# Optimization experiments

Measured on AMD Instinct MI355X. Metric: run time of the kernel, lower is better.

Reference implementation:

```python
import jax, jax.numpy as jnp
import numpy as np

BLOCK_NUM = 1024

def setup_inputs() -> dict:
    key = jax.random.key(0)
    k1, k2 = jax.random.split(key)
    regional_means = jax.random.normal(k1, (32, BLOCK_NUM, 128), dtype=jnp.float32)
    adj = jax.random.uniform(k2, (32, BLOCK_NUM, BLOCK_NUM), dtype=jnp.float32)
    return {"regional_means": regional_means, "adj": adj}

def reference(regional_means, adj):
    # Original: adj_means[b,i,j,f] = adj[b,i,j] * regional_means[b,j,f],
    # diagonal (i==j) zeroed, then summed over j.
    # Algebraically: (adj with zeroed diagonal) @ regional_means.
    n = adj.shape[-1]
    mask = 1.0 - jnp.eye(n, dtype=adj.dtype)  # (n, n)
    adj_masked = adj * mask  # (b, n, n)
    # (b, n, n) @ (b, n, f) -> (b, n, f)
    return jnp.einsum('bij,bjf->bif', adj_masked, regional_means)
```

## Files before the change

kernel.cpp:

```cpp
#include <hip/hip_runtime.h>
#include <hip/hip_bf16.h>
#include <stdint.h>

typedef __attribute__((ext_vector_type(4))) float f32x4;
typedef __attribute__((ext_vector_type(2))) float f32x2;
typedef __attribute__((ext_vector_type(8))) short short8;
typedef __attribute__((ext_vector_type(4))) unsigned int u32x4;

__device__ __forceinline__ unsigned short f2bf(float x) {
  __hip_bfloat16 h = __float2bfloat16(x);
  union { __hip_bfloat16 b; unsigned short s; } u; u.b = h;
  return u.s;
}
__device__ __forceinline__ unsigned int pkbf(float lo, float hi) {
  return (unsigned int)f2bf(lo) | ((unsigned int)f2bf(hi) << 16);
}
__device__ __forceinline__ f32x4 ld4(const float* p) { return *(const f32x4*)p; }


#define MSK(v, k) (((k) == arow) ? 0.f : (v))

#define LOADA(kt, Aa, Ab, Ac, Ad) do {                                  \
    const float* p_ = aP + (kt) * 64;                                   \
    Aa = ld4(p_); Ab = ld4(p_ + 4); Ac = ld4(p_ + 32); Ad = ld4(p_ + 36); \
  } while (0)

#define LOADB(kt, B_) do {                                              \
    const f32x2* p_ = (const f32x2*)(bP + (size_t)(kt) * 8192);         \
    _Pragma("unroll") for (int e_ = 0; e_ < 8; ++e_) B_[e_] = p_[e_ * 64]; \
  } while (0)

#define STAGEB(buf, B_) do {                                            \
    u32x4 ua_, ub_;                                                     \
    ua_[0] = pkbf(B_[0].x, B_[1].x); ua_[1] = pkbf(B_[2].x, B_[3].x);   \
    ua_[2] = pkbf(B_[4].x, B_[5].x); ua_[3] = pkbf(B_[6].x, B_[7].x);   \
    ub_[0] = pkbf(B_[0].y, B_[1].y); ub_[1] = pkbf(B_[2].y, B_[3].y);   \
    ub_[2] = pkbf(B_[4].y, B_[5].y); ub_[3] = pkbf(B_[6].y, B_[7].y);   \
    char* p_ = wP + (buf) * 16384;                                      \
    *(u32x4*)p_ = ua_; *(u32x4*)(p_ + 16) = ub_;                        \
  } while (0)

#define COMPUTE(buf, kt, Aa, Ab, Ac, Ad) do {                           \
    short8 af0_, af1_;                                                  \
    {                                                                   \
      union { u32x4 q; short8 s; } u0_, u1_;                            \
      if ((kt) == diag_kt) {  \
        const int jb_ = (kt) * 64 + kg;                                 \
        u0_.q[0] = pkbf(MSK(Aa[0], jb_ + 0),  MSK(Aa[1], jb_ + 1));     \
        u0_.q[1] = pkbf(MSK(Aa[2], jb_ + 2),  MSK(Aa[3], jb_ + 3));     \
        u0_.q[2] = pkbf(MSK(Ab[0], jb_ + 4),  MSK(Ab[1], jb_ + 5));     \
        u0_.q[3] = pkbf(MSK(Ab[2], jb_ + 6),  MSK(Ab[3], jb_ + 7));     \
        u1_.q[0] = pkbf(MSK(Ac[0], jb_ + 32), MSK(Ac[1], jb_ + 33));    \
        u1_.q[1] = pkbf(MSK(Ac[2], jb_ + 34), MSK(Ac[3], jb_ + 35));    \
        u1_.q[2] = pkbf(MSK(Ad[0], jb_ + 36), MSK(Ad[1], jb_ + 37));    \
        u1_.q[3] = pkbf(MSK(Ad[2], jb_ + 38), MSK(Ad[3], jb_ + 39));    \
      } else {                                                          \
        u0_.q[0] = pkbf(Aa[0], Aa[1]); u0_.q[1] = pkbf(Aa[2], Aa[3]);   \
        u0_.q[2] = pkbf(Ab[0], Ab[1]); u0_.q[3] = pkbf(Ab[2], Ab[3]);   \
        u1_.q[0] = pkbf(Ac[0], Ac[1]); u1_.q[1] = pkbf(Ac[2], Ac[3]);   \
        u1_.q[2] = pkbf(Ad[0], Ad[1]); u1_.q[3] = pkbf(Ad[2], Ad[3]);   \
      }                                                                 \
      af0_ = u0_.s; af1_ = u1_.s;                                       \
    }                                                                   \
    const char* base_ = rP + (buf) * 16384;                             \
    _Pragma("unroll")                                                   \
    for (int n_ = 0; n_ < 8; ++n_) {                                    \
      short8 bf0_ = *(const short8*)(base_ + (n_ * 2 + 0) * 1024);      \
      acc[n_] = __builtin_amdgcn_mfma_f32_16x16x32_bf16(af0_, bf0_, acc[n_], 0, 0, 0); \
      short8 bf1_ = *(const short8*)(base_ + (n_ * 2 + 1) * 1024);      \
      acc[n_] = __builtin_amdgcn_mfma_f32_16x16x32_bf16(af1_, bf1_, acc[n_], 0, 0, 0); \
    }                                                                   \
  } while (0)

__global__ __launch_bounds__(512) void gcn_kernel(
    const float* __restrict__ means, const float* __restrict__ adj,
    float* __restrict__ out) {
  __shared__ char ldsB[32768];

  const int tid = (int)threadIdx.x;
  const int l = tid & 63;
  const int w = tid >> 6;
  const int bid = (int)blockIdx.x;
  const int batch = (bid & 7) * 4 + (bid >> 6);
  const int rtile = (bid >> 3) & 7;
  const int rbase = rtile * 128;

  const float* aB = adj + (size_t)batch * 1048576;
  const float* mB = means + (size_t)batch * 131072;
  float* oB = out + (size_t)batch * 131072;

  const int arow = rbase + w * 16 + (l & 15);
  const int kg = (l >> 4) * 8;
  const float* aP = aB + (size_t)arow * 1024 + kg;
  const int diag_kt = arow >> 6;

  const int n_t = tid >> 6;
  const int s_t = (tid >> 5) & 1;
  const int g_t = (tid >> 3) & 3;
  const int fc_t = (tid & 7) * 2;
  const float* bP = mB + (size_t)(s_t * 32 + g_t * 8) * 128 + n_t * 16 + fc_t;

  char* wP = ldsB + tid * 32;
  const char* rP = ldsB + l * 16;

  f32x4 acc[8];
#pragma unroll
  for (int n = 0; n < 8; ++n) { f32x4 z = {0.f, 0.f, 0.f, 0.f}; acc[n] = z; }

  f32x4 A00, A01, A02, A03, A10, A11, A12, A13;
  f32x2 B0v[8], B1v[8];

  LOADA(0, A00, A01, A02, A03);
  LOADB(0, B0v);
  STAGEB(0, B0v);
  __syncthreads();

  for (int kt = 0; kt < 16; kt += 2) {
    LOADA(kt + 1, A10, A11, A12, A13);
    LOADB(kt + 1, B1v);
    COMPUTE(0, kt, A00, A01, A02, A03);
    STAGEB(1, B1v);
    __syncthreads();

    if (kt + 2 < 16) {
      LOADA(kt + 2, A00, A01, A02, A03);
      LOADB(kt + 2, B0v);
    }
    COMPUTE(1, kt + 1, A10, A11, A12, A13);
    if (kt + 2 < 16) STAGEB(0, B0v);
    __syncthreads();
  }

  const int orow = rbase + w * 16 + (l >> 4) * 4;
  const int ocol = l & 15;
  float* op = oB + (size_t)orow * 128 + ocol;
#pragma unroll
  for (int n = 0; n < 8; ++n)
#pragma unroll
    for (int j = 0; j < 4; ++j)
      op[j * 128 + n * 16] = acc[n][j];
}

extern "C" void kernel_launch(void* const* d_in, const int* in_sizes, int n_in,
                              void* d_out, int out_size, void* d_ws, size_t ws_size,
                              hipStream_t stream) {
  const float* means = (const float*)d_in[0];
  const float* adj = (const float*)d_in[1];
  float* out = (float*)d_out;
  hipLaunchKernelGGL(gcn_kernel, dim3(256), dim3(512), 0, stream, means, adj, out);
}
```

Before: 216.8 us.

## Halve row tile to 64 rows, 512 blocks, stage B in 128-k chunks

Cuts the row tile per block from 128 to 64 and the threads per block from 512 to 256, launching 512 blocks with launch bounds targeting two blocks per CU. The B operand (means) is staged into LDS in 128-deep k chunks across a 64KB double buffer, with one barrier per two k-steps instead of two per two. The aim is better CU fill on 256 CUs and less synchronisation, in exchange for each block re-reading the means matrix twice as often and doubling LDS use, which may limit occupancy.

After: 216.4 us. Within noise of the previous version (-0.2%).

```diff
diff --git a/kernel.cpp b/kernel.cpp
--- a/kernel.cpp
+++ b/kernel.cpp
@@ -20,70 +20,73 @@
 
 #define MSK(v, k) (((k) == arow) ? 0.f : (v))
 
-#define LOADA(kt, Aa, Ab, Ac, Ad) do {                                  \
-    const float* p_ = aP + (kt) * 64;                                   \
-    Aa = ld4(p_); Ab = ld4(p_ + 4); Ac = ld4(p_ + 32); Ad = ld4(p_ + 36); \
+#define LOADA(kt, Aq) do {                                               \
+    const float* p_ = aP + (kt) * 64;                                    \
+    Aq[0] = ld4(p_); Aq[1] = ld4(p_ + 4);                                \
+    Aq[2] = ld4(p_ + 32); Aq[3] = ld4(p_ + 36);                          \
   } while (0)
 
-#define LOADB(kt, B_) do {                                              \
-    const f32x2* p_ = (const f32x2*)(bP + (size_t)(kt) * 8192);         \
-    _Pragma("unroll") for (int e_ = 0; e_ < 8; ++e_) B_[e_] = p_[e_ * 64]; \
+#define STAGE_LOAD(q1, h, S_) do {                                       \
+    const float* p_ = bP0 + (q1) * 16384 + (h) * 4096;                   \
+    _Pragma("unroll") for (int e_ = 0; e_ < 8; ++e_)                     \
+      S_[e_] = *(const f32x2*)(p_ + e_ * 128);                           \
   } while (0)
 
-#define STAGEB(buf, B_) do {                                            \
-    u32x4 ua_, ub_;                                                     \
-    ua_[0] = pkbf(B_[0].x, B_[1].x); ua_[1] = pkbf(B_[2].x, B_[3].x);   \
-    ua_[2] = pkbf(B_[4].x, B_[5].x); ua_[3] = pkbf(B_[6].x, B_[7].x);   \
-    ub_[0] = pkbf(B_[0].y, B_[1].y); ub_[1] = pkbf(B_[2].y, B_[3].y);   \
-    ub_[2] = pkbf(B_[4].y, B_[5].y); ub_[3] = pkbf(B_[6].y, B_[7].y);   \
-    char* p_ = wP + (buf) * 16384;                                      \
-    *(u32x4*)p_ = ua_; *(u32x4*)(p_ + 16) = ub_;                        \
+#define STAGE_WRITE(nb, h, S_) do {                                      \
+    u32x4 ua_, ub_;                                                      \
+    ua_[0] = pkbf(S_[0].x, S_[1].x); ua_[1] = pkbf(S_[2].x, S_[3].x);    \
+    ua_[2] = pkbf(S_[4].x, S_[5].x); ua_[3] = pkbf(S_[6].x, S_[7].x);    \
+    ub_[0] = pkbf(S_[0].y, S_[1].y); ub_[1] = pkbf(S_[2].y, S_[3].y);    \
+    ub_[2] = pkbf(S_[4].y, S_[5].y); ub_[3] = pkbf(S_[6].y, S_[7].y);    \
+    char* p_ = wB + (nb) * 32768 + (h) * 1024;                           \
+    *(u32x4*)p_ = ua_; *(u32x4*)(p_ + 16) = ub_;                         \
   } while (0)
 
-#define COMPUTE(buf, kt, Aa, Ab, Ac, Ad) do {                           \
-    short8 af0_, af1_;                                                  \
-    {                                                                   \
-      union { u32x4 q; short8 s; } u0_, u1_;                            \
-      if ((kt) == diag_kt) {  \
-        const int jb_ = (kt) * 64 + kg;                                 \
-        u0_.q[0] = pkbf(MSK(Aa[0], jb_ + 0),  MSK(Aa[1], jb_ + 1));     \
-        u0_.q[1] = pkbf(MSK(Aa[2], jb_ + 2),  MSK(Aa[3], jb_ + 3));     \
-        u0_.q[2] = pkbf(MSK(Ab[0], jb_ + 4),  MSK(Ab[1], jb_ + 5));     \
-        u0_.q[3] = pkbf(MSK(Ab[2], jb_ + 6),  MSK(Ab[3], jb_ + 7));     \
-        u1_.q[0] = pkbf(MSK(Ac[0], jb_ + 32), MSK(Ac[1], jb_ + 33));    \
-        u1_.q[1] = pkbf(MSK(Ac[2], jb_ + 34), MSK(Ac[3], jb_ + 35));    \
-        u1_.q[2] = pkbf(MSK(Ad[0], jb_ + 36), MSK(Ad[1], jb_ + 37));    \
-        u1_.q[3] = pkbf(MSK(Ad[2], jb_ + 38), MSK(Ad[3], jb_ + 39));    \
-      } else {                                                          \
-        u0_.q[0] = pkbf(Aa[0], Aa[1]); u0_.q[1] = pkbf(Aa[2], Aa[3]);   \
-        u0_.q[2] = pkbf(Ab[0], Ab[1]); u0_.q[3] = pkbf(Ab[2], Ab[3]);   \
-        u1_.q[0] = pkbf(Ac[0], Ac[1]); u1_.q[1] = pkbf(Ac[2], Ac[3]);   \
-        u1_.q[2] = pkbf(Ad[0], Ad[1]); u1_.q[3] = pkbf(Ad[2], Ad[3]);   \
-      }                                                                 \
-      af0_ = u0_.s; af1_ = u1_.s;                                       \
-    }                                                                   \
-    const char* base_ = rP + (buf) * 16384;                             \
-    _Pragma("unroll")                                                   \
-    for (int n_ = 0; n_ < 8; ++n_) {                                    \
-      short8 bf0_ = *(const short8*)(base_ + (n_ * 2 + 0) * 1024);      \
+#define COMPUTE(buf, kt, Aq) do {                                        \
+    short8 af0_, af1_;                                                   \
+    {                                                                    \
+      union { u32x4 q; short8 s; } u0_, u1_;                             \
+      if ((kt) == diag_kt) {                                             \
+        const int jb_ = (kt) * 64 + kg;                                  \
+        u0_.q[0] = pkbf(MSK(Aq[0][0], jb_ + 0),  MSK(Aq[0][1], jb_ + 1)); \
+        u0_.q[1] = pkbf(MSK(Aq[0][2], jb_ + 2),  MSK(Aq[0][3], jb_ + 3)); \
+        u0_.q[2] = pkbf(MSK(Aq[1][0], jb_ + 4),  MSK(Aq[1][1], jb_ + 5)); \
+        u0_.q[3] = pkbf(MSK(Aq[1][2], jb_ + 6),  MSK(Aq[1][3], jb_ + 7)); \
+        u1_.q[0] = pkbf(MSK(Aq[2][0], jb_ + 32), MSK(Aq[2][1], jb_ + 33)); \
+        u1_.q[1] = pkbf(MSK(Aq[2][2], jb_ + 34), MSK(Aq[2][3], jb_ + 35)); \
+        u1_.q[2] = pkbf(MSK(Aq[3][0], jb_ + 36), MSK(Aq[3][1], jb_ + 37)); \
+        u1_.q[3] = pkbf(MSK(Aq[3][2], jb_ + 38), MSK(Aq[3][3], jb_ + 39)); \
+      } else {                                                           \
+        u0_.q[0] = pkbf(Aq[0][0], Aq[0][1]); u0_.q[1] = pkbf(Aq[0][2], Aq[0][3]); \
+        u0_.q[2] = pkbf(Aq[1][0], Aq[1][1]); u0_.q[3] = pkbf(Aq[1][2], Aq[1][3]); \
+        u1_.q[0] = pkbf(Aq[2][0], Aq[2][1]); u1_.q[1] = pkbf(Aq[2][2], Aq[2][3]); \
+        u1_.q[2] = pkbf(Aq[3][0], Aq[3][1]); u1_.q[3] = pkbf(Aq[3][2], Aq[3][3]); \
+      }                                                                  \
+      af0_ = u0_.s; af1_ = u1_.s;                                        \
+    }                                                                    \
+    const char* base_ = rP + (buf) * 32768;                              \
+    const int c_ = (kt) & 1;                                             \
+    _Pragma("unroll")                                                    \
+    for (int n_ = 0; n_ < 8; ++n_) {                                     \
+      short8 bf0_ = *(const short8*)(base_ + (n_ * 4 + 2 * c_ + 0) * 1024); \
       acc[n_] = __builtin_amdgcn_mfma_f32_16x16x32_bf16(af0_, bf0_, acc[n_], 0, 0, 0); \
-      short8 bf1_ = *(const short8*)(base_ + (n_ * 2 + 1) * 1024);      \
+      short8 bf1_ = *(const short8*)(base_ + (n_ * 4 + 2 * c_ + 1) * 1024); \
       acc[n_] = __builtin_amdgcn_mfma_f32_16x16x32_bf16(af1_, bf1_, acc[n_], 0, 0, 0); \
-    }                                                                   \
+    }                                                                    \
   } while (0)
 
-__global__ __launch_bounds__(512) void gcn_kernel(
+__global__ __launch_bounds__(256, 2) void gcn_kernel(
     const float* __restrict__ means, const float* __restrict__ adj,
     float* __restrict__ out) {
-  __shared__ char ldsB[32768];
+  __shared__ char ldsB[65536];
 
   const int tid = (int)threadIdx.x;
   const int l = tid & 63;
   const int w = tid >> 6;
   const int bid = (int)blockIdx.x;
-  const int batch = (bid & 7) * 4 + (bid >> 6);
-  const int rtile = (bid >> 3) & 7;
-  const int rbase = rtile * 128;
+  const int batch = (bid & 7) * 4 + (bid >> 7);
+  const int rtile = (bid >> 3) & 15;
+  const int rbase = rtile * 64;
 
   const float* aB = adj + (size_t)batch * 1048576;
   const float* mB = means + (size_t)batch * 131072;
@@ -94,41 +97,53 @@
   const float* aP = aB + (size_t)arow * 1024 + kg;
   const int diag_kt = arow >> 6;
 
-  const int n_t = tid >> 6;
-  const int s_t = (tid >> 5) & 1;
+  const int n_t = tid >> 5;
   const int g_t = (tid >> 3) & 3;
   const int fc_t = (tid & 7) * 2;
-  const float* bP = mB + (size_t)(s_t * 32 + g_t * 8) * 128 + n_t * 16 + fc_t;
-
-  char* wP = ldsB + tid * 32;
+  const float* bP0 = mB + (size_t)(g_t * 8) * 128 + n_t * 16 + fc_t;
+  char* wB = ldsB + n_t * 4096 + g_t * 256 + fc_t * 16;
   const char* rP = ldsB + l * 16;
 
   f32x4 acc[8];
 #pragma unroll
   for (int n = 0; n < 8; ++n) { f32x4 z = {0.f, 0.f, 0.f, 0.f}; acc[n] = z; }
 
-  f32x4 A00, A01, A02, A03, A10, A11, A12, A13;
-  f32x2 B0v[8], B1v[8];
+  f32x4 Ar[2][4];
 
-  LOADA(0, A00, A01, A02, A03);
-  LOADB(0, B0v);
-  STAGEB(0, B0v);
+  {
+    f32x2 S0[8], S1[8], S2[8], S3[8];
+    STAGE_LOAD(0, 0, S0); STAGE_LOAD(0, 1, S1);
+    STAGE_LOAD(0, 2, S2); STAGE_LOAD(0, 3, S3);
+    LOADA(0, Ar[0]);
+    STAGE_WRITE(0, 0, S0); STAGE_WRITE(0, 1, S1);
+    STAGE_WRITE(0, 2, S2); STAGE_WRITE(0, 3, S3);
+  }
   __syncthreads();
 
-  for (int kt = 0; kt < 16; kt += 2) {
-    LOADA(kt + 1, A10, A11, A12, A13);
-    LOADB(kt + 1, B1v);
-    COMPUTE(0, kt, A00, A01, A02, A03);
-    STAGEB(1, B1v);
-    __syncthreads();
+#pragma unroll
+  for (int kt = 0; kt < 16; ++kt) {
+    const int q = kt >> 1;
+    const int c = kt & 1;
+    const int buf = q & 1;
+    const int nbuf = buf ^ 1;
+    const int cur = kt & 1;
+    const int nxt = cur ^ 1;
 
-    if (kt + 2 < 16) {
-      LOADA(kt + 2, A00, A01, A02, A03);
-      LOADB(kt + 2, B0v);
+    if (kt < 15) LOADA(kt + 1, Ar[nxt]);
+
+    f32x2 S0[8], S1[8];
+    if (q < 7) {
+      STAGE_LOAD(q + 1, 2 * c + 0, S0);
+      STAGE_LOAD(q + 1, 2 * c + 1, S1);
     }
-    COMPUTE(1, kt + 1, A10, A11, A12, A13);
-    if (kt + 2 < 16) STAGEB(0, B0v);
-    __syncthreads();
+
+    COMPUTE(buf, kt, Ar[cur]);
+
+    if (q < 7) {
+      STAGE_WRITE(nbuf, 2 * c + 0, S0);
+      STAGE_WRITE(nbuf, 2 * c + 1, S1);
+    }
+    if (c == 1) __syncthreads();
   }
 
   const int orow = rbase + w * 16 + (l >> 4) * 4;
@@ -147,5 +162,5 @@
   const float* means = (const float*)d_in[0];
   const float* adj = (const float*)d_in[1];
   float* out = (float*)d_out;
-  hipLaunchKernelGGL(gcn_kernel, dim3(256), dim3(512), 0, stream, means, adj, out);
+  hipLaunchKernelGGL(gcn_kernel, dim3(512), dim3(256), 0, stream, means, adj, out);
 }
```
